# Performance work log

Hardware: AMD Instinct MI355X
Metric: run time of the kernel (lower is better)

## Reference

```python
import math
import jax, jax.numpy as jnp
from jax import lax
import numpy as np

C = 256; A = 3; NIMG = 2; L = 5
SIZES = [(200, 304), (100, 152), (50, 76), (25, 38), (13, 19)]
STRIDES = [4, 8, 16, 32, 64]
LVTOP = 600          # cfg['lvtop'] (eval)
IMTOP = 300          # cfg['imtop1'] (eval)
SCORE_THR = 0.0      # cfg['score_thr1']
MIN_SIZE = 1e-2      # cfg['min_size1']
IOU_THR = 0.7        # cfg['iou_thr1']
IMH, IMW = 800.0, 1216.0
BBOX_CLIP = math.log(1000.0 / 16.0)   # clamp=True in decode_boxes
GROUP_OFF = 4096.0                     # > max canvas coord -> disjoint NMS groups


def _level_anchors(h, w, stride):
    scale = stride * 8.0
    r = np.array([0.5, 1.0, 2.0])
    ws = scale * np.sqrt(r); hs = scale / np.sqrt(r)          # [A]
    ys, xs = np.meshgrid(np.arange(h), np.arange(w), indexing='ij')
    cx = (xs.reshape(-1, 1) + 0.5) * stride                    # [HW,1]
    cy = (ys.reshape(-1, 1) + 0.5) * stride
    a = np.stack([cx - ws / 2, cy - hs / 2, cx + ws / 2, cy + hs / 2], axis=-1)
    return a.reshape(-1, 4).astype(np.float32)                 # [HW*A,4]


def setup_inputs() -> dict:
    key = jax.random.key(0)
    ks = jax.random.split(key, 10)
    inp = {}
    for i, (h, w) in enumerate(SIZES):
        inp[f'fmap{i}'] = jax.random.normal(ks[i], (NIMG, C, h, w), jnp.float32)
        inp[f'priors{i}'] = jnp.asarray(_level_anchors(h, w, STRIDES[i]))
    inp['imsizes'] = jnp.array([[IMH, IMW]] * NIMG, jnp.float32)   # (h, w) per image
    inp['conv_w'] = jax.random.normal(ks[5], (C, C, 3, 3), jnp.float32) * 0.03
    inp['conv_b'] = jnp.zeros((C,), jnp.float32)
    inp['log_w'] = jax.random.normal(ks[6], (A, C), jnp.float32) * 0.03
    inp['log_b'] = jnp.zeros((A,), jnp.float32)
    inp['reg_w'] = jax.random.normal(ks[7], (A * 4, C), jnp.float32) * 0.01
    inp['reg_b'] = jnp.zeros((A * 4,), jnp.float32)
    return inp


def _decode(reg, pri):
    pw = pri[..., 2] - pri[..., 0]; ph = pri[..., 3] - pri[..., 1]
    pcx = pri[..., 0] + 0.5 * pw;   pcy = pri[..., 1] + 0.5 * ph
    dx, dy = reg[..., 0], reg[..., 1]
    dw = jnp.minimum(reg[..., 2], BBOX_CLIP)
    dh = jnp.minimum(reg[..., 3], BBOX_CLIP)
    cx = dx * pw + pcx; cy = dy * ph + pcy
    w = pw * jnp.exp(dw); h = ph * jnp.exp(dh)
    return jnp.stack([cx - 0.5 * w, cy - 0.5 * h, cx + 0.5 * w, cy + 0.5 * h], axis=-1)


def _forward(fmaps, priors, imsizes, conv_w, conv_b, log_w, log_b, reg_w, reg_b):
    dn = ('NCHW', 'OIHW', 'NCHW')
    boxes_l, score_l = [], []
    for x, pri in zip(fmaps, priors):
        n = x.shape[0]
        h = jax.nn.relu(lax.conv_general_dilated(x, conv_w, (1, 1), 'SAME',
                                                 dimension_numbers=dn)
                        + conv_b[None, :, None, None])
        logit = (jnp.einsum('nchw,ac->nahw', h, log_w)
                 + log_b[None, :, None, None]).transpose(0, 2, 3, 1).reshape(n, -1)
        reg = (jnp.einsum('nchw,ac->nahw', h, reg_w)
               + reg_b[None, :, None, None]).transpose(0, 2, 3, 1).reshape(n, -1, 4)
        vals, top = lax.top_k(logit, LVTOP)                        # per-level topk
        reg_g = jnp.take_along_axis(reg, jnp.broadcast_to(top[:, :, None], (n, LVTOP, 4)), axis=1)
        pri_g = pri[top]                                           # [n,k,4]
        boxes_l.append(_decode(reg_g, pri_g))
        score_l.append(jax.nn.sigmoid(vals))
    boxes = jnp.concatenate(boxes_l, axis=1)                       # [n, L*k, 4]
    obj = jnp.concatenate(score_l, axis=1)                         # [n, L*k]
    n, dim = boxes.shape[0], boxes.shape[1]
    Nall = n * dim
    boxes = boxes.reshape(Nall, 4); obj = obj.reshape(Nall)
    imidx = jnp.arange(Nall) // dim
    lvl = jnp.tile(jnp.repeat(jnp.arange(L), LVTOP), n)
    valid = obj >= SCORE_THR
    sz = imsizes[imidx]                                            # [Nall,2] (h,w)
    boxes = jnp.stack([jnp.clip(boxes[:, 0], 0.0, sz[:, 1]),
                       jnp.clip(boxes[:, 1], 0.0, sz[:, 0]),
                       jnp.clip(boxes[:, 2], 0.0, sz[:, 1]),
                       jnp.clip(boxes[:, 3], 0.0, sz[:, 0])], axis=-1)
    valid = valid & (boxes[:, 2] - boxes[:, 0] >= MIN_SIZE) & (boxes[:, 3] - boxes[:, 1] >= MIN_SIZE)
    groups = imidx * 10 + lvl                                      # batched_nms groups
    # sort by score, invalid entries pushed to the end
    order = jnp.argsort(-jnp.where(valid, obj, -1.0))
    b = boxes[order]; v = valid[order]; g = groups[order]; im = imidx[order]
    # group-offset trick == torchvision batched_nms
    ob = b + g.astype(b.dtype)[:, None] * GROUP_OFF
    area = (ob[:, 2] - ob[:, 0]) * (ob[:, 3] - ob[:, 1])
    lt = jnp.maximum(ob[:, None, :2], ob[None, :, :2])
    rb = jnp.minimum(ob[:, None, 2:], ob[None, :, 2:])
    wh = jnp.maximum(rb - lt, 0.0)
    inter = wh[..., 0] * wh[..., 1]
    iou = lax.stop_gradient(inter / (area[:, None] + area[None, :] - inter))
    idxr = jnp.arange(Nall)
    def body(i, keep):
        sup = jnp.any(keep & (iou[i] > IOU_THR) & (idxr < i))
        return keep.at[i].set(v[i] & ~sup)
    keep = lax.fori_loop(0, Nall, body, jnp.zeros((Nall,), bool))
    # per-image cap at IMTOP (keep is already in score order)
    sel = keep[None, :] & (im[None, :] == jnp.arange(n)[:, None])  # [n,Nall]
    sel = sel & (jnp.cumsum(sel, axis=1) <= IMTOP)
    prio = jnp.where(sel, Nall - idxr[None, :], 0)
    pvals, pos = lax.top_k(prio, IMTOP)                            # [n,IMTOP]
    vout = pvals > 0
    bout = jnp.where(vout[..., None], b[pos], 0.0)                 # [n,IMTOP,4]
    imout = jnp.broadcast_to(jnp.arange(n)[:, None], (n, IMTOP)).reshape(-1).astype(jnp.int32)
    return bout.reshape(-1, 4), imout, vout.reshape(-1)


def reference(fmap0, fmap1, fmap2, fmap3, fmap4,
              priors0, priors1, priors2, priors3, priors4,
              imsizes, conv_w, conv_b, log_w, log_b, reg_w, reg_b):
    return _forward([fmap0, fmap1, fmap2, fmap3, fmap4],
                    [priors0, priors1, priors2, priors3, priors4],
                    imsizes, conv_w, conv_b, log_w, log_b, reg_w, reg_b)
```

## Files before the change

### kernel.cpp

```cpp
#include <hip/hip_runtime.h>
#include <math.h>

typedef unsigned long long u64;
typedef unsigned int u32;
typedef unsigned short u16;
typedef _Float16 f16;
typedef __attribute__((ext_vector_type(8))) _Float16 f16x8;
typedef __attribute__((ext_vector_type(8))) unsigned short ushort8;
typedef __attribute__((ext_vector_type(4))) float f32x4;

#define LVTOP 600
#define IMTOP 300
#define NIMG 2
#define NLVL 5
#define NCAND (NLVL*LVTOP)

__constant__ int d_HW[5]    = {60800,15200,3800,950,247};
__constant__ int d_LGOFF[5] = {0,364800,456000,478800,484500};
__constant__ int d_RGOFF[5] = {0,1459200,1824000,1915200,1938000};
__constant__ int d_H[5]  = {200,100,50,25,13};
__constant__ int d_W[5]  = {304,152,76,38,19};
__constant__ int d_TX[5] = {7,4,2,1,1};
__constant__ long d_XB[5] = {0, 31129600, 38912000, 40857600, 41344000};
__constant__ long d_CB[5] = {0, 3891200, 4864000, 5107200, 5168000};
__constant__ int d_SB[6] = {0,64,80,84,85,86};
#define NCHUNK 5183808
#define WS_NEED 178889200ull

__device__ __forceinline__ u32 okey(float f){
  u32 u = __float_as_uint(f);
  return (u & 0x80000000u) ? ~u : (u | 0x80000000u);
}

__device__ __forceinline__ void f16_split(float v, u16& hb, u16& lb){
  f16 h = (f16)v;
  float r = v - (float)h;
  f16 l = (f16)r;
  hb = __builtin_bit_cast(u16, h);
  lb = __builtin_bit_cast(u16, l);
}

__device__ __forceinline__ u64 shfl64(u64 v, int src){
  u32 lo = __shfl((u32)v, src);
  u32 hi = __shfl((u32)(v >> 32), src);
  return ((u64)hi << 32) | lo;
}

__device__ __forceinline__ void dma16(const u16* g, u16* l){
  __builtin_amdgcn_global_load_lds(
      (const __attribute__((address_space(1))) u32*)g,
      (__attribute__((address_space(3))) u32*)l, 16, 0, 0);
}

template<int NN, int NT>
__device__ void bitonic_desc64(u64* a, int tid){
  for (int k = 2; k <= NN; k <<= 1){
    for (int j = k >> 1; j > 0; j >>= 1){
      __syncthreads();
      for (int i = tid; i < NN; i += NT){
        int ixj = i ^ j;
        if (ixj > i){
          u64 x = a[i], y = a[ixj];
          bool up = ((i & k) == 0);
          if (up ? (x < y) : (x > y)){ a[i] = y; a[ixj] = x; }
        }
      }
    }
  }
  __syncthreads();
}

template<int NN, int NT>
__device__ void bitonic_asc32(u32* a, int tid){
  for (int k = 2; k <= NN; k <<= 1){
    for (int j = k >> 1; j > 0; j >>= 1){
      __syncthreads();
      for (int i = tid; i < NN; i += NT){
        int ixj = i ^ j;
        if (ixj > i){
          u32 x = a[i], y = a[ixj];
          bool up = ((i & k) == 0);
          if (up ? (x > y) : (x < y)){ a[i] = y; a[ixj] = x; }
        }
      }
    }
  }
  __syncthreads();
}

__device__ void suffix_scan(u32* s, int NB, int tid){
  for (int off = 1; off < NB; off <<= 1){
    u32 v0 = 0, v1 = 0;
    int i1 = tid + 1024;
    if (tid < NB) v0 = s[tid] + ((tid + off < NB) ? s[tid + off] : 0u);
    if (i1  < NB) v1 = s[i1]  + ((i1  + off < NB) ? s[i1  + off] : 0u);
    __syncthreads();
    if (tid < NB) s[tid] = v0;
    if (i1  < NB) s[i1]  = v1;
    __syncthreads();
  }
}

__global__ __launch_bounds__(256) void wprep(
    const float* __restrict__ cw, const float* __restrict__ lw,
    const float* __restrict__ rw, u16* __restrict__ wT, u16* __restrict__ whB,
    u32* __restrict__ ghist)
{
  int t = threadIdx.x;
  if (blockIdx.x < 72){
    int id = blockIdx.x*256 + t;
    int cc = id & 7;
    int co = (id >> 3) & 255;
    int tap = id >> 11;
    int ntg = co >> 4;
    size_t base = (size_t)((tap*8 + cc)*16 + ntg) * 1024;
    #pragma unroll
    for (int ci = 0; ci < 32; ci++){
      float v = cw[(size_t)co*2304 + (size_t)(cc*32 + ci)*9 + tap];
      u16 hi, lo; f16_split(v, hi, lo);
      int q = ci >> 3, j = ci & 7;
      int lane = q*16 + (co & 15);
      wT[base + lane*8 + j] = hi;
      wT[base + 512 + lane*8 + j] = lo;
    }
  } else if (blockIdx.x == 72){
    if (t < 128){
      int ks = t >> 4, nn = t & 15;
      for (int ci = 0; ci < 32; ci++){
        int k = ks*32 + ci;
        float v = 0.0f;
        if (nn < 3) v = lw[nn*256 + k];
        else if (nn < 15) v = rw[(nn-3)*256 + k];
        u16 hi, lo; f16_split(v, hi, lo);
        int q = ci >> 3, j = ci & 7;
        int lane = q*16 + nn;
        whB[ks*1024 + lane*8 + j] = hi;
        whB[ks*1024 + 512 + lane*8 + j] = lo;
      }
    }
  } else {
    int z = (blockIdx.x - 73)*1024 + t;
    #pragma unroll
    for (int q = 0; q < 4; q++){
      int i = z + q*256;
      if (i < NLVL*NIMG*2048) ghist[i] = 0;
    }
  }
}

__global__ __launch_bounds__(256) void xsplit(
    const float* __restrict__ f0, const float* __restrict__ f1,
    const float* __restrict__ f2, const float* __restrict__ f3,
    const float* __restrict__ f4,
    u16* __restrict__ xh, u16* __restrict__ xl, u16* __restrict__ zp)
{
  long id = (long)blockIdx.x*256 + threadIdx.x;
  if (blockIdx.x == 0 && threadIdx.x < 8) zp[threadIdx.x] = 0;
  if (id >= NCHUNK) return;
  int l = (id < d_CB[1]) ? 0 : (id < d_CB[2]) ? 1 : (id < d_CB[3]) ? 2 : (id < d_CB[4]) ? 3 : 4;
  long rem = id - d_CB[l];
  int HW = d_HW[l];
  int n = (int)(rem / (32*HW));
  int r2 = (int)(rem - (long)n*32*HW);
  int cg = r2 / HW;
  int p = r2 - cg*HW;
  const float* fm = (l==0)?f0:(l==1)?f1:(l==2)?f2:(l==3)?f3:f4;
  const float* gp = fm + ((size_t)(n*256 + cg*8))*HW + p;
  ushort8 hv, lv;
  #pragma unroll
  for (int j = 0; j < 8; j++){
    float v = gp[(size_t)j*HW];
    u16 hb, lb; f16_split(v, hb, lb);
    hv[j] = hb; lv[j] = lb;
  }
  *(ushort8*)&xh[id*8] = hv;
  *(ushort8*)&xl[id*8] = lv;
}

__global__ __launch_bounds__(256, 2) void conv_mfma(
    const float* __restrict__ f0, const float* __restrict__ f1,
    const float* __restrict__ f2, const float* __restrict__ f3,
    const float* __restrict__ f4,
    const u16* __restrict__ xh, const u16* __restrict__ xl,
    const u16* __restrict__ zp,
    const u16* __restrict__ wT, const u16* __restrict__ whB,
    const float* __restrict__ cb, const float* __restrict__ lb,
    const float* __restrict__ rb,
    float* __restrict__ lgb, float* __restrict__ rgb, int use_dma)
{
  __shared__ __align__(16) u16 smem[26624];

  const int t = threadIdx.x;
  const int n = blockIdx.y;
  int bx = blockIdx.x;
  int l, rbk;
  if (bx < 700){ l = 0; rbk = bx; }
  else if (bx < 900){ l = 1; rbk = bx - 700; }
  else if (bx < 950){ l = 2; rbk = bx - 900; }
  else if (bx < 963){ l = 3; rbk = bx - 950; }
  else { l = 4; rbk = bx - 963; }
  const int H = d_H[l], W = d_W[l], tilesX = d_TX[l];
  const int ty2 = rbk / tilesX;
  const int x0 = (rbk - ty2*tilesX) * 48;
  const float* fm = (l==0) ? f0 : (l==1) ? f1 : (l==2) ? f2 : (l==3) ? f3 : f4;

  const int wave = t >> 6, lane = t & 63;
  const int quad = lane >> 4, l15 = lane & 15;
  const int HWp = H * W;
  const float* xin = fm + (size_t)n * 256 * HWp;

  f32x4 acc[2][3][4];
  #pragma unroll
  for (int r = 0; r < 2; r++)
    #pragma unroll
    for (int a = 0; a < 3; a++)
      #pragma unroll
      for (int b = 0; b < 4; b++) acc[r][a][b] = (f32x4){0.f,0.f,0.f,0.f};

  auto compute_cc = [&](int cc, int bufo){
    #pragma unroll
    for (int ky = 0; ky < 3; ky++){
      #pragma unroll
      for (int kx = 0; kx < 3; kx++){
        const u16* bt = wT + (size_t)((((ky*3+kx)*8 + cc)*16) + wave*4) * 1024 + lane*8;
        f16x8 Bh[4], Bl[4];
        #pragma unroll
        for (int nt = 0; nt < 4; nt++){
          Bh[nt] = *(const f16x8*)(bt + nt*1024);
          Bl[nt] = *(const f16x8*)(bt + nt*1024 + 512);
        }
        #pragma unroll
        for (int row = 0; row < 2; row++){
          int o0 = bufo + ((quad*4 + ky + row)*52 + (l15 + kx))*8;
          f16x8 Ah[3], Al[3];
          #pragma unroll
          for (int mt = 0; mt < 3; mt++){
            Ah[mt] = *(const f16x8*)&smem[o0 + mt*128];
            Al[mt] = *(const f16x8*)&smem[o0 + 6656 + mt*128];
          }
          #pragma unroll
          for (int nt = 0; nt < 4; nt++){
            #pragma unroll
            for (int mt = 0; mt < 3; mt++){
              acc[row][mt][nt] = __builtin_amdgcn_mfma_f32_16x16x32_f16(Ah[mt], Bh[nt], acc[row][mt][nt], 0,0,0);
              acc[row][mt][nt] = __builtin_amdgcn_mfma_f32_16x16x32_f16(Al[mt], Bh[nt], acc[row][mt][nt], 0,0,0);
              acc[row][mt][nt] = __builtin_amdgcn_mfma_f32_16x16x32_f16(Ah[mt], Bl[nt], acc[row][mt][nt], 0,0,0);
            }
          }
        }
      }
    }
  };

  if (use_dma){
    const u16* ph[4]; const u16* pl[4]; u32 pstep[4]; int dsth[4]; int kv[4];
    #pragma unroll
    for (int s = 0; s < 4; s++){
      int k = wave + s*4;
      kv[s] = (k < 13);
      int kk = kv[s] ? k : 0;
      int g = kk*64 + lane;
      int cg = g / 208; int rem = g - cg*208;
      int r = rem / 52;  int xi = rem - r*52;
      int gy = ty2*2 - 1 + r, gx = x0 - 1 + xi;
      bool inb = (gy >= 0) && (gy < H) && (gx >= 0) && (gx < W);
      int gy2 = gy < 0 ? 0 : (gy >= H ? H-1 : gy);
      int gx2 = gx < 0 ? 0 : (gx >= W ? W-1 : gx);
      long off = d_XB[l] + (((long)(n*32 + cg))*HWp + (long)gy2*W + gx2)*8;
      ph[s] = inb ? (xh + off) : zp;
      pl[s] = inb ? (xl + off) : zp;
      pstep[s] = inb ? (u32)(32*HWp) : 0u;
      dsth[s] = kk*512;
    }
    auto stage = [&](int bufo){
      #pragma unroll
      for (int s = 0; s < 4; s++){
        if (kv[s]){
          dma16(ph[s], &smem[bufo + dsth[s]]);
          dma16(pl[s], &smem[bufo + 6656 + dsth[s]]);
          ph[s] += pstep[s]; pl[s] += pstep[s];
        }
      }
    };
    stage(0);
    __syncthreads();
    for (int cc = 0; cc < 8; cc++){
      if (cc < 7) stage(((cc+1)&1)*13312);
      compute_cc(cc, (cc&1)*13312);
      __syncthreads();
    }
  } else {
    for (int cc = 0; cc < 8; cc++){
      __syncthreads();
      #pragma unroll
      for (int it = 0; it < 4; it++){
        int G = t + it*256;
        if (G < 832){
          int cg = G / 208; int rem = G - cg*208;
          int r = rem / 52; int xi = rem - r*52;
          int gy = ty2*2 - 1 + r, gx = x0 - 1 + xi;
          bool inb = (gy >= 0) & (gy < H) & (gx >= 0) & (gx < W);
          const float* gp = xin + (size_t)(cc*32 + cg*8) * HWp
                          + (size_t)(gy < 0 ? 0 : gy) * W + (gx < 0 ? 0 : gx);
          ushort8 hv, lv;
          #pragma unroll
          for (int j = 0; j < 8; j++){
            float v = inb ? gp[(size_t)j * HWp] : 0.0f;
            u16 hb, lb2; f16_split(v, hb, lb2);
            hv[j] = hb; lv[j] = lb2;
          }
          int off = G*8;
          *(ushort8*)&smem[off] = hv;
          *(ushort8*)&smem[6656 + off] = lv;
        }
      }
      __syncthreads();
      compute_cc(cc, 0);
    }
    __syncthreads();
  }

  u16* hA_h = smem;
  u16* hA_l = smem + 8704;
  #pragma unroll
  for (int row = 0; row < 2; row++){
    const int ty = ty2*2 + row;
    const bool rowok = (ty < H);
    if (rowok){
      f32x4 a2 = (f32x4){0.f,0.f,0.f,0.f};
      #pragma unroll
      for (int half = 0; half < 2; half++){
        if ((wave >> 1) == half){
          #pragma unroll
          for (int mt = 0; mt < 3; mt++){
            #pragma unroll
            for (int nt = 0; nt < 4; nt++){
              int col = (wave & 1)*64 + nt*16 + l15;
              float bias = cb[half*128 + col];
              #pragma unroll
              for (int r = 0; r < 4; r++){
                float h = fmaxf(acc[row][mt][nt][r] + bias, 0.0f);
                u16 hb, lb2; f16_split(h, hb, lb2);
                int pos = mt*16 + quad*4 + r;
                hA_h[pos*136 + col] = hb;
                hA_l[pos*136 + col] = lb2;
              }
            }
          }
        }
        __syncthreads();
        #pragma unroll
        for (int ks2 = 0; ks2 < 4; ks2++){
          int ks = half*4 + ks2;
          int ao = (wave*16 + l15)*136 + ks2*32 + quad*8;
          f16x8 Ah = *(const f16x8*)&hA_h[ao];
          f16x8 Al = *(const f16x8*)&hA_l[ao];
          const u16* wb = whB + ks*1024 + lane*8;
          f16x8 Bh = *(const f16x8*)wb;
          f16x8 Bl = *(const f16x8*)(wb + 512);
          a2 = __builtin_amdgcn_mfma_f32_16x16x32_f16(Ah, Bh, a2, 0,0,0);
          a2 = __builtin_amdgcn_mfma_f32_16x16x32_f16(Al, Bh, a2, 0,0,0);
          a2 = __builtin_amdgcn_mfma_f32_16x16x32_f16(Ah, Bl, a2, 0,0,0);
        }
        __syncthreads();
      }

      float* sm_out = (float*)smem;
      {
        int o = l15;
        float bias = (o < 3) ? lb[o] : ((o < 15) ? rb[o-3] : 0.0f);
        #pragma unroll
        for (int r = 0; r < 4; r++){
          int pos = wave*16 + quad*4 + r;
          sm_out[pos*16 + o] = a2[r] + bias;
        }
      }
      __syncthreads();
      {
        int P = W - x0; if (P > 48) P = 48;
        size_t pbase = (size_t)ty * W + x0;
        float* lg = lgb + d_LGOFF[l] + (size_t)n*HWp*3  + pbase*3;
        float* rg = rgb + d_RGOFF[l] + (size_t)n*HWp*12 + pbase*12;
        for (int j = t; j < P*3; j += 256)  lg[j] = sm_out[(j/3)*16 + (j%3)];
        for (int j = t; j < P*12; j += 256) rg[j] = sm_out[(j/12)*16 + 3 + (j%12)];
      }
      __syncthreads();
    }
  }
}

__global__ __launch_bounds__(256) void hist1(
    const float* __restrict__ lg, u32* __restrict__ ghist)
{
  __shared__ u32 lh[2048];
  int t = threadIdx.x;
  int b = blockIdx.x, n = blockIdx.y;
  int l = (b < d_SB[1]) ? 0 : (b < d_SB[2]) ? 1 : (b < d_SB[3]) ? 2 : (b < d_SB[4]) ? 3 : 4;
  int s = b - d_SB[l], nsl = d_SB[l+1] - d_SB[l];
  int N = d_HW[l] * 3;
  const float* lgl = lg + d_LGOFF[l] + (size_t)n * N;
  for (int i = t; i < 2048; i += 256) lh[i] = 0;
  __syncthreads();
  int lo = (int)((long)N * s / nsl), hi = (int)((long)N * (s+1) / nsl);
  for (int i = lo + t; i < hi; i += 256)
    atomicAdd(&lh[okey(lgl[i]) >> 21], 1u);
  __syncthreads();
  u32* gh = ghist + (size_t)(l*NIMG + n) * 2048;
  for (int i = t; i < 2048; i += 256)
    if (lh[i]) atomicAdd(&gh[i], lh[i]);
}

__global__ __launch_bounds__(1024) void topk_decode(
    const float* __restrict__ lg, const float* __restrict__ rg,
    const float* __restrict__ pr0, const float* __restrict__ pr1,
    const float* __restrict__ pr2, const float* __restrict__ pr3,
    const float* __restrict__ pr4,
    const float* __restrict__ imsizes, const u32* __restrict__ ghist,
    float* __restrict__ cbox, float* __restrict__ cscore, u32* __restrict__ cvalid)
{
  __shared__ u32 hist[2048];
  __shared__ u32 sscan[2048];
  __shared__ u64 sel[1024];
  __shared__ u32 eqbuf[1024];
  __shared__ u32 scal[8];
  int tid = threadIdx.x;
  int l = blockIdx.x / NIMG;
  int n = blockIdx.x - l*NIMG;
  int HW = d_HW[l];
  int N = HW * 3;
  const float* lgl = lg + d_LGOFF[l] + (size_t)n * N;

  {
    const u32* gh = ghist + (size_t)blockIdx.x * 2048;
    for (int i = tid; i < 2048; i += 1024){ u32 h = gh[i]; hist[i] = h; sscan[i] = h; }
  }
  __syncthreads();
  suffix_scan(sscan, 2048, tid);
  if (tid < 2048){
    u32 Si = sscan[tid], Sn = (tid+1 < 2048) ? sscan[tid+1] : 0u;
    if (Si >= LVTOP && Sn < LVTOP){ scal[0] = (u32)tid; scal[1] = Si - hist[tid]; }
  }
  { int i2 = tid + 1024;
    u32 Si = sscan[i2], Sn = (i2+1 < 2048) ? sscan[i2+1] : 0u;
    if (Si >= LVTOP && Sn < LVTOP){ scal[0] = (u32)i2; scal[1] = Si - hist[i2]; } }
  __syncthreads();
  u32 B1 = scal[0], base1 = scal[1];

  for (int i = tid; i < 2048; i += 1024) hist[i] = 0;
  __syncthreads();
  for (int i = tid; i < N; i += 1024){
    u32 k = okey(lgl[i]);
    if ((k >> 21) == B1) atomicAdd(&hist[(k >> 10) & 0x7FFu], 1u);
  }
  __syncthreads();
  for (int i = tid; i < 2048; i += 1024) sscan[i] = hist[i];
  __syncthreads();
  suffix_scan(sscan, 2048, tid);
  {
    u32 need = LVTOP - base1;
    if (tid < 2048){
      u32 Si = sscan[tid], Sn = (tid+1 < 2048) ? sscan[tid+1] : 0u;
      if (Si >= need && Sn < need){ scal[2] = (u32)tid; scal[3] = base1 + Si - hist[tid]; }
    }
    int i2 = tid + 1024;
    u32 Si = sscan[i2], Sn = (i2+1 < 2048) ? sscan[i2+1] : 0u;
    if (Si >= need && Sn < need){ scal[2] = (u32)i2; scal[3] = base1 + Si - hist[i2]; }
  }
  __syncthreads();
  u32 B2 = scal[2], base2 = scal[3];

  for (int i = tid; i < 1024; i += 1024) hist[i] = 0;
  __syncthreads();
  u32 hi21 = (B1 << 11) | B2;
  for (int i = tid; i < N; i += 1024){
    u32 k = okey(lgl[i]);
    if ((k >> 10) == hi21) atomicAdd(&hist[k & 0x3FFu], 1u);
  }
  __syncthreads();
  for (int i = tid; i < 1024; i += 1024) sscan[i] = hist[i];
  __syncthreads();
  suffix_scan(sscan, 1024, tid);
  {
    u32 need = LVTOP - base2;
    if (tid < 1024){
      u32 Si = sscan[tid], Sn = (tid+1 < 1024) ? sscan[tid+1] : 0u;
      if (Si >= need && Sn < need){
        scal[4] = (hi21 << 10) | (u32)tid;
        scal[5] = base2 + Si - hist[tid];
      }
    }
  }
  if (tid == 0){ scal[6] = 0; scal[7] = 0; }
  __syncthreads();
  u32 T = scal[4], nAbove = scal[5], needEq = LVTOP - scal[5];

  for (int i = tid; i < 1024; i += 1024) sel[i] = 0;
  __syncthreads();
  for (int i = tid; i < N; i += 1024){
    u32 k = okey(lgl[i]);
    if (k > T){
      u32 p = atomicAdd(&scal[6], 1u);
      sel[p] = ((u64)k << 32) | (0xFFFFFFFFu - (u32)i);
    } else if (k == T){
      u32 p = atomicAdd(&scal[7], 1u);
      if (p < 1024) eqbuf[p] = (u32)i;
    }
  }
  __syncthreads();
  u32 cntE = scal[7];
  if (cntE > needEq){
    u32 m = cntE < 1024u ? cntE : 1024u;
    for (int i = tid; i < 1024; i += 1024) if ((u32)i >= m) eqbuf[i] = 0xFFFFFFFFu;
    __syncthreads();
    bitonic_asc32<1024,1024>(eqbuf, tid);
  }
  __syncthreads();
  if ((u32)tid < needEq)
    sel[nAbove + tid] = ((u64)T << 32) | (0xFFFFFFFFu - eqbuf[tid]);
  __syncthreads();
  bitonic_desc64<1024,1024>(sel, tid);

  if (tid < LVTOP){
    u64 c = sel[tid];
    u32 i = 0xFFFFFFFFu - (u32)c;
    float val = lgl[i];
    float score = 1.0f / (1.0f + expf(-val));
    int pp = (int)i / 3, a = (int)i - pp*3;
    const float* pri;
    if (l == 0) pri = pr0; else if (l == 1) pri = pr1; else if (l == 2) pri = pr2;
    else if (l == 3) pri = pr3; else pri = pr4;
    pri += (size_t)i * 4;
    const float* rgp = rg + d_RGOFF[l] + ((size_t)n * HW + pp) * 12 + a * 4;
    float px0 = pri[0], py0 = pri[1], px1 = pri[2], py1 = pri[3];
    float pw = px1 - px0, ph = py1 - py0;
    float pcx = px0 + 0.5f*pw, pcy = py0 + 0.5f*ph;
    const float BC = (float)4.135166556742356;
    float dx = rgp[0], dy = rgp[1];
    float dw = fminf(rgp[2], BC), dh = fminf(rgp[3], BC);
    float cx = dx*pw + pcx, cy = dy*ph + pcy;
    float bw = pw * expf(dw), bh = ph * expf(dh);
    float x1 = cx - 0.5f*bw, y1 = cy - 0.5f*bh;
    float x2 = cx + 0.5f*bw, y2 = cy + 0.5f*bh;
    float imh = imsizes[n*2+0], imw = imsizes[n*2+1];
    x1 = fminf(fmaxf(x1, 0.0f), imw);
    y1 = fminf(fmaxf(y1, 0.0f), imh);
    x2 = fminf(fmaxf(x2, 0.0f), imw);
    y2 = fminf(fmaxf(y2, 0.0f), imh);
    u32 valid = (score >= 0.0f) && ((x2 - x1) >= 1e-2f) && ((y2 - y1) >= 1e-2f);
    int ci = n*NCAND + l*LVTOP + tid;
    cbox[ci*4+0] = x1; cbox[ci*4+1] = y1; cbox[ci*4+2] = x2; cbox[ci*4+3] = y2;
    cscore[ci] = score; cvalid[ci] = valid;
  }
}

__global__ __launch_bounds__(1024) void sort_cand(
    const float* __restrict__ cscore, const u32* __restrict__ cvalid,
    const float* __restrict__ cbox,
    float* __restrict__ sbox, float* __restrict__ sob,
    float* __restrict__ sarea, u32* __restrict__ svalid,
    u32* __restrict__ rlist, u32* __restrict__ kflag)
{
  __shared__ u64 a[4096];
  int tid = threadIdx.x, n = blockIdx.x;
  for (int i = tid; i < 4096; i += 1024){
    if (i < NCAND){
      int ci = n*NCAND + i;
      float s = cvalid[ci] ? cscore[ci] : -1.0f;
      a[i] = ((u64)okey(s) << 32) | (0xFFFFFFFFu - (u32)i);
    } else a[i] = 0;
  }
  bitonic_desc64<4096,1024>(a, tid);
  int mylvl[3];
  #pragma unroll
  for (int q = 0; q < 3; q++){
    int r = tid + q*1024;
    mylvl[q] = 0;
    if (r < NCAND){
      u32 li = 0xFFFFFFFFu - (u32)a[r];
      int ci = n*NCAND + (int)li;
      float b0 = cbox[ci*4+0], b1 = cbox[ci*4+1], b2 = cbox[ci*4+2], b3 = cbox[ci*4+3];
      int lvl = (int)li / LVTOP;
      mylvl[q] = lvl;
      float off = (float)(n*10 + lvl) * 4096.0f;
      int so = n*NCAND + r;
      sbox[so*4+0]=b0; sbox[so*4+1]=b1; sbox[so*4+2]=b2; sbox[so*4+3]=b3;
      float o0=b0+off, o1=b1+off, o2=b2+off, o3=b3+off;
      sob[so*4+0]=o0; sob[so*4+1]=o1; sob[so*4+2]=o2; sob[so*4+3]=o3;
      sarea[so] = (o2-o0)*(o3-o1);
      svalid[so] = cvalid[ci];
    }
  }
  __syncthreads();
  #pragma unroll
  for (int q = 0; q < 3; q++){
    int r = tid + q*1024;
    a[r] = (r < NCAND) ? (1ull << (12*mylvl[q])) : 0ull;
  }
  a[tid + 3072] = 0ull;
  __syncthreads();
  for (int off = 1; off < 4096; off <<= 1){
    u64 v[4];
    #pragma unroll
    for (int q = 0; q < 4; q++){
      int i = tid + q*1024;
      v[q] = a[i] + ((i >= off) ? a[i-off] : 0ull);
    }
    __syncthreads();
    #pragma unroll
    for (int q = 0; q < 4; q++) a[tid + q*1024] = v[q];
    __syncthreads();
  }
  #pragma unroll
  for (int q = 0; q < 3; q++){
    int r = tid + q*1024;
    if (r < NCAND){
      int lv = mylvl[q];
      int pos = (int)((a[r] >> (12*lv)) & 0xFFFull) - 1;
      rlist[(n*NLVL + lv)*LVTOP + pos] = (u32)r;
      kflag[n*NCAND + r] = 0u;
    }
  }
}

__global__ __launch_bounds__(256) void nms_mask_l(
    const float* __restrict__ sob, const float* __restrict__ sarea,
    const u32* __restrict__ svalid, const u32* __restrict__ rlist,
    u64* __restrict__ pmask)
{
  __shared__ float sj[64*5];
  int tid = threadIdx.x;
  int nl = blockIdx.y;
  int n = nl / NLVL;
  int i = blockIdx.x*256 + tid;
  bool act = false;
  float oi0=0, oi1=0, oi2=0, oi3=0, ai=0;
  if (i < LVTOP){
    int so = n*NCAND + (int)rlist[nl*LVTOP + i];
    act = svalid[so] != 0;
    oi0 = sob[so*4+0]; oi1 = sob[so*4+1]; oi2 = sob[so*4+2]; oi3 = sob[so*4+3];
    ai = sarea[so];
  }
  for (int w = 0; w < 10; w++){
    __syncthreads();
    if (tid < 64){
      int j = w*64 + tid;
      if (j < LVTOP){
        int so = n*NCAND + (int)rlist[nl*LVTOP + j];
        sj[tid*5+0]=sob[so*4+0]; sj[tid*5+1]=sob[so*4+1];
        sj[tid*5+2]=sob[so*4+2]; sj[tid*5+3]=sob[so*4+3];
        sj[tid*5+4]=sarea[so];
      }
    }
    __syncthreads();
    if (act){
      u64 bits = 0;
      int jj0 = (i >= w*64) ? (i - w*64 + 1) : 0;
      int jjend = (LVTOP - w*64 < 64) ? (LVTOP - w*64) : 64;
      for (int jj = jj0; jj < jjend; jj++){
        float oj0=sj[jj*5+0], oj1=sj[jj*5+1], oj2=sj[jj*5+2], oj3=sj[jj*5+3], aj=sj[jj*5+4];
        float ltx = fmaxf(oi0, oj0), lty = fmaxf(oi1, oj1);
        float rbx = fminf(oi2, oj2), rby = fminf(oi3, oj3);
        float wx = fmaxf(rbx - ltx, 0.0f), wy = fmaxf(rby - lty, 0.0f);
        float inter = wx * wy;
        float iou = inter / ((ai + aj) - inter);
        if (iou > 0.7f) bits |= (1ull << jj);
      }
      pmask[((size_t)(nl*LVTOP + i))*10 + w] = bits;
    }
  }
}

__global__ __launch_bounds__(256) void nms_scan_l(
    const u64* __restrict__ pmask, const u32* __restrict__ svalid,
    const u32* __restrict__ rlist, u32* __restrict__ kflag)
{
  __shared__ u64 pm[LVTOP*10];
  int t = threadIdx.x, nl = blockIdx.x, n = nl / NLVL;
  const u64* gpm = pmask + (size_t)nl * LVTOP * 10;
  for (int i = t; i < LVTOP*10; i += 256) pm[i] = gpm[i];
  __syncthreads();
  if (t < 64){
    u64 vw = 0, remv = 0;
    for (int c = 0; c < 10; c++){
      int i = c*64 + t;
      int pred = 0;
      if (i < LVTOP) pred = svalid[n*NCAND + (int)rlist[nl*LVTOP + i]] != 0;
      u64 b = __ballot(pred);
      if (t == c) vw = b;
    }
    for (int w = 0; w < 10; w++){
      u64 act = shfl64(vw, w) & ~shfl64(remv, w);
      while (act){
        int bpos = __builtin_ctzll(act);
        int i = w*64 + bpos;
        if (t == 0) kflag[n*NCAND + (int)rlist[nl*LVTOP + i]] = 1u;
        u64 m = (t < 10) ? pm[i*10 + t] : 0ull;
        u64 mw = pm[i*10 + w];
        remv |= m;
        act &= ~(1ull << bpos);
        act &= ~mw;
      }
    }
  }
}

__global__ __launch_bounds__(1024) void merge_out(
    const u32* __restrict__ kflag, const float* __restrict__ sbox,
    float* __restrict__ out)
{
  __shared__ u32 ps[4096];
  int tid = threadIdx.x, n = blockIdx.x;
  u32 f[4];
  #pragma unroll
  for (int q = 0; q < 4; q++){
    int i = tid + q*1024;
    f[q] = (i < NCAND) ? kflag[n*NCAND + i] : 0u;
    ps[i] = f[q];
  }
  __syncthreads();
  for (int off = 1; off < 4096; off <<= 1){
    u32 v[4];
    #pragma unroll
    for (int q = 0; q < 4; q++){
      int i = tid + q*1024;
      v[q] = ps[i] + ((i >= off) ? ps[i-off] : 0u);
    }
    __syncthreads();
    #pragma unroll
    for (int q = 0; q < 4; q++) ps[tid + q*1024] = v[q];
    __syncthreads();
  }
  #pragma unroll
  for (int q = 0; q < 4; q++){
    int i = tid + q*1024;
    if (i < NCAND && f[q] && ps[i] <= IMTOP){
      int slot = n*IMTOP + (int)ps[i] - 1;
      int so = n*NCAND + i;
      out[slot*4+0] = sbox[so*4+0]; out[slot*4+1] = sbox[so*4+1];
      out[slot*4+2] = sbox[so*4+2]; out[slot*4+3] = sbox[so*4+3];
    }
  }
  u32 kept = ps[NCAND-1]; if (kept > IMTOP) kept = IMTOP;
  for (int j = tid; j < IMTOP; j += 1024){
    int slot = n*IMTOP + j;
    if ((u32)j >= kept){
      out[slot*4+0]=0; out[slot*4+1]=0; out[slot*4+2]=0; out[slot*4+3]=0;
    }
    out[2400 + slot] = (float)n;
    out[3000 + slot] = ((u32)j < kept) ? 1.0f : 0.0f;
  }
}

extern "C" void kernel_launch(void* const* d_in, const int* in_sizes, int n_in,
                              void* d_out, int out_size, void* d_ws, size_t ws_size,
                              hipStream_t stream)
{
  const float* fmap[5]   = {(const float*)d_in[0], (const float*)d_in[2], (const float*)d_in[4],
                            (const float*)d_in[6], (const float*)d_in[8]};
  const float* priors[5] = {(const float*)d_in[1], (const float*)d_in[3], (const float*)d_in[5],
                            (const float*)d_in[7], (const float*)d_in[9]};
  const float* imsz   = (const float*)d_in[10];
  const float* conv_w = (const float*)d_in[11];
  const float* conv_b = (const float*)d_in[12];
  const float* log_w  = (const float*)d_in[13];
  const float* log_b  = (const float*)d_in[14];
  const float* reg_w  = (const float*)d_in[15];
  const float* reg_b  = (const float*)d_in[16];

  char* base = (char*)d_ws;
  float* lg     = (float*)(base + 0);
  float* rg     = (float*)(base + 1943928);
  float* cscore = (float*)(base + 9719640);
  float* cbox   = (float*)(base + 9743640);
  u32*   cvalid = (u32*)  (base + 9839640);
  float* sbox   = (float*)(base + 9863640);
  float* sob    = (float*)(base + 9959640);
  float* sarea  = (float*)(base + 10055640);
  u32*   svalid = (u32*)  (base + 10079640);
  u32*   rlist  = (u32*)  (base + 10103640);
  u32*   kflag  = (u32*)  (base + 10127640);
  u64*   pmask  = (u64*)  (base + 10151648);
  u32*   ghist  = (u32*)  (base + 10151648);
  u16*   wT     = (u16*)  (base + 10631648);
  u16*   whB    = (u16*)  (base + 12990944);
  u16*   zp     = (u16*)  (base + 13007328);
  u16*   xh     = (u16*)  (base + 13007344);
  u16*   xl     = (u16*)  (base + 95948272);

  int use_dma = (ws_size >= WS_NEED) ? 1 : 0;

  wprep<<<93, 256, 0, stream>>>(conv_w, log_w, reg_w, wT, whB, ghist);
  if (use_dma)
    xsplit<<<(NCHUNK + 255)/256, 256, 0, stream>>>(
        fmap[0], fmap[1], fmap[2], fmap[3], fmap[4], xh, xl, zp);

  conv_mfma<<<dim3(970, NIMG), 256, 0, stream>>>(
      fmap[0], fmap[1], fmap[2], fmap[3], fmap[4],
      xh, xl, zp, wT, whB, conv_b, log_b, reg_b, lg, rg, use_dma);

  hist1<<<dim3(86, NIMG), 256, 0, stream>>>(lg, ghist);

  topk_decode<<<NLVL*NIMG, 1024, 0, stream>>>(lg, rg,
      priors[0], priors[1], priors[2], priors[3], priors[4],
      imsz, ghist, cbox, cscore, cvalid);
  sort_cand<<<NIMG, 1024, 0, stream>>>(cscore, cvalid, cbox, sbox, sob, sarea,
                                       svalid, rlist, kflag);
  nms_mask_l<<<dim3(3, NIMG*NLVL), 256, 0, stream>>>(sob, sarea, svalid, rlist, pmask);
  nms_scan_l<<<NIMG*NLVL, 256, 0, stream>>>(pmask, svalid, rlist, kflag);
  merge_out<<<NIMG, 1024, 0, stream>>>(kflag, sbox, (float*)d_out);
}
```

Baseline: 1.118 ms.

## Fuse logit histogram into conv epilogue and replace bitonic sort with rank sort

The separate hist1 kernel is removed. Each conv block now builds a shared-memory histogram of its logit keys while writing logits, then flushes it to the global histogram with atomics. This saves a kernel launch and a full re-read of the logit buffer, at the cost of extra shared atomics and a global flush in every conv block. The 1024-element bitonic sort in topk_decode is replaced by a counting rank sort in which each thread compares against all keys. That assumes keys are unique, which holds because the low bits encode the index, but padding entries may be duplicates.

```diff
diff --git a/kernel.cpp b/kernel.cpp
--- a/kernel.cpp
+++ b/kernel.cpp
@@ -23,7 +23,6 @@
 __constant__ int d_TX[5] = {7,4,2,1,1};
 __constant__ long d_XB[5] = {0, 31129600, 38912000, 40857600, 41344000};
 __constant__ long d_CB[5] = {0, 3891200, 4864000, 5107200, 5168000};
-__constant__ int d_SB[6] = {0,64,80,84,85,86};
 #define NCHUNK 5183808
 #define WS_NEED 178889200ull
 
@@ -186,7 +185,8 @@
     const u16* __restrict__ wT, const u16* __restrict__ whB,
     const float* __restrict__ cb, const float* __restrict__ lb,
     const float* __restrict__ rb,
-    float* __restrict__ lgb, float* __restrict__ rgb, int use_dma)
+    float* __restrict__ lgb, float* __restrict__ rgb,
+    u32* __restrict__ ghist, int use_dma)
 {
   __shared__ __align__(16) u16 smem[26624];
 
@@ -319,6 +319,9 @@
     }
     __syncthreads();
   }
+
+  u32* lhist = (u32*)(smem + 17408);
+  for (int i = t; i < 2048; i += 256) lhist[i] = 0;
 
   u16* hA_h = smem;
   u16* hA_l = smem + 8704;
@@ -381,33 +384,24 @@
         size_t pbase = (size_t)ty * W + x0;
         float* lg = lgb + d_LGOFF[l] + (size_t)n*HWp*3  + pbase*3;
         float* rg = rgb + d_RGOFF[l] + (size_t)n*HWp*12 + pbase*12;
-        for (int j = t; j < P*3; j += 256)  lg[j] = sm_out[(j/3)*16 + (j%3)];
+        for (int j = t; j < P*3; j += 256){
+          float v = sm_out[(j/3)*16 + (j%3)];
+          lg[j] = v;
+          atomicAdd(&lhist[okey(v) >> 21], 1u);
+        }
         for (int j = t; j < P*12; j += 256) rg[j] = sm_out[(j/12)*16 + 3 + (j%12)];
       }
       __syncthreads();
     }
   }
-}
-
-__global__ __launch_bounds__(256) void hist1(
-    const float* __restrict__ lg, u32* __restrict__ ghist)
-{
-  __shared__ u32 lh[2048];
-  int t = threadIdx.x;
-  int b = blockIdx.x, n = blockIdx.y;
-  int l = (b < d_SB[1]) ? 0 : (b < d_SB[2]) ? 1 : (b < d_SB[3]) ? 2 : (b < d_SB[4]) ? 3 : 4;
-  int s = b - d_SB[l], nsl = d_SB[l+1] - d_SB[l];
-  int N = d_HW[l] * 3;
-  const float* lgl = lg + d_LGOFF[l] + (size_t)n * N;
-  for (int i = t; i < 2048; i += 256) lh[i] = 0;
-  __syncthreads();
-  int lo = (int)((long)N * s / nsl), hi = (int)((long)N * (s+1) / nsl);
-  for (int i = lo + t; i < hi; i += 256)
-    atomicAdd(&lh[okey(lgl[i]) >> 21], 1u);
-  __syncthreads();
-  u32* gh = ghist + (size_t)(l*NIMG + n) * 2048;
-  for (int i = t; i < 2048; i += 256)
-    if (lh[i]) atomicAdd(&gh[i], lh[i]);
+
+  {
+    u32* gh = ghist + (size_t)(l*NIMG + n) * 2048;
+    for (int i = t; i < 2048; i += 256){
+      u32 h = lhist[i];
+      if (h) atomicAdd(&gh[i], h);
+    }
+  }
 }
 
 __global__ __launch_bounds__(1024) void topk_decode(
@@ -518,7 +512,14 @@
   if ((u32)tid < needEq)
     sel[nAbove + tid] = ((u64)T << 32) | (0xFFFFFFFFu - eqbuf[tid]);
   __syncthreads();
-  bitonic_desc64<1024,1024>(sel, tid);
+  {
+    u64 mykey = sel[tid];
+    int rank = 0;
+    for (int j = 0; j < 1024; j++) rank += (sel[j] > mykey) ? 1 : 0;
+    __syncthreads();
+    sel[rank] = mykey;
+  }
+  __syncthreads();
 
   if (tid < LVTOP){
     u64 c = sel[tid];
@@ -796,9 +797,7 @@
 
   conv_mfma<<<dim3(970, NIMG), 256, 0, stream>>>(
       fmap[0], fmap[1], fmap[2], fmap[3], fmap[4],
-      xh, xl, zp, wT, whB, conv_b, log_b, reg_b, lg, rg, use_dma);
-
-  hist1<<<dim3(86, NIMG), 256, 0, stream>>>(lg, ghist);
+      xh, xl, zp, wT, whB, conv_b, log_b, reg_b, lg, rg, ghist, use_dma);
 
   topk_decode<<<NLVL*NIMG, 1024, 0, stream>>>(lg, rg,
       priors[0], priors[1], priors[2], priors[3], priors[4],
```

Result: no change. 1.124 ms (+0.5%).
